# Optimization experiments

Hardware: AMD Instinct MI355X
Metric: run time of the kernel (lower is better)

The kernel has to match this reference:

```python
import jax, jax.numpy as jnp
import numpy as np

H = 4          # heads
C = 64         # per-head channels
HID = 256      # hidden_dim = H*C
L = 4          # num_layers
N = 50000      # nodes
E = 300000     # edges
G = 64         # graphs
NODE_DIMS = [80, 16, 8]
EDGE_DIMS = [8, 4]


def setup_inputs() -> dict:
    key = jax.random.key(0)
    ks = iter(jax.random.split(key, 64))
    def nrm(shape, fan_in):
        return jax.random.normal(next(ks), shape, dtype=jnp.float32) * (1.0 / np.sqrt(fan_in))
    inp = {}
    inp['x'] = jax.random.randint(next(ks), (N, 3), 0, 8)
    inp['edge_attr'] = jax.random.randint(next(ks), (E, 2), 0, 4)
    inp['edge_index'] = jax.random.randint(next(ks), (2, E), 0, N)
    inp['batch'] = jnp.sort(jax.random.randint(next(ks), (N,), 0, G))
    inp['scalars'] = jax.random.uniform(next(ks), (G, 5), dtype=jnp.float32)
    inp['num_graphs'] = G
    # categorical embedding tables (summed per field)
    inp['node_emb0'] = nrm((NODE_DIMS[0], HID), HID)
    inp['node_emb1'] = nrm((NODE_DIMS[1], HID), HID)
    inp['node_emb2'] = nrm((NODE_DIMS[2], HID), HID)
    inp['edge_emb0'] = nrm((EDGE_DIMS[0], HID), HID)
    inp['edge_emb1'] = nrm((EDGE_DIMS[1], HID), HID)
    # stacked per-layer TransformerConv params
    inp['Wq'] = nrm((L, HID, HID), HID); inp['bq'] = jnp.zeros((L, HID))
    inp['Wk'] = nrm((L, HID, HID), HID); inp['bk'] = jnp.zeros((L, HID))
    inp['Wv'] = nrm((L, HID, HID), HID); inp['bv'] = jnp.zeros((L, HID))
    inp['We'] = nrm((L, HID, HID), HID); inp['be'] = jnp.zeros((L, HID))
    inp['Wskip'] = nrm((L, HID, HID), HID); inp['bskip'] = jnp.zeros((L, HID))
    inp['Wbeta'] = nrm((L, 3 * HID, 1), 3 * HID)  # beta gate, bias=False in PyG
    inp['ln_g'] = jnp.ones((L, HID)); inp['ln_b'] = jnp.zeros((L, HID))
    # pragma scalar encoder
    inp['pw1'] = nrm((5, HID), 5); inp['pb1'] = jnp.zeros((HID,))
    inp['pw2'] = nrm((HID, HID), HID); inp['pb2'] = jnp.zeros((HID,))
    # readout MLP
    inp['rw1'] = nrm((HID, HID), HID); inp['rb1'] = jnp.zeros((HID,))
    inp['rw2'] = nrm((HID, HID // 2), HID); inp['rb2'] = jnp.zeros((HID // 2,))
    inp['rw3'] = nrm((HID // 2, 4), HID // 2); inp['rb3'] = jnp.zeros((4,))
    return inp


def _forward(scalars, node_emb0, node_emb1, node_emb2, edge_emb0, edge_emb1,
             Wq, bq, Wk, bk, Wv, bv, We, be, Wskip, bskip, Wbeta, ln_g, ln_b,
             pw1, pb1, pw2, pb2, rw1, rb1, rw2, rb2, rw3, rb3,
             x, edge_attr, edge_index, batch, num_graphs):
    n = x.shape[0]
    src, dst = edge_index[0], edge_index[1]
    # CategoricalEmbedding: sum of per-field embeddings
    h = node_emb0[x[:, 0]] + node_emb1[x[:, 1]] + node_emb2[x[:, 2]]      # [N, HID]
    ef = edge_emb0[edge_attr[:, 0]] + edge_emb1[edge_attr[:, 1]]          # [E, HID]
    scale = 1.0 / jnp.sqrt(jnp.asarray(C, h.dtype))
    for l in range(L):
        q = (h @ Wq[l] + bq[l]).reshape(n, H, C)
        kN = (h @ Wk[l] + bk[l]).reshape(n, H, C)
        vN = (h @ Wv[l] + bv[l]).reshape(n, H, C)
        e = (ef @ We[l] + be[l]).reshape(-1, H, C)                        # [E, H, C]
        kj = kN[src] + e                                                  # edge feat added to keys
        alpha = jnp.sum(q[dst] * kj, axis=-1) * scale                     # [E, H]
        # segment softmax over incoming edges per destination node
        amax = jax.ops.segment_max(alpha, dst, num_segments=n)
        amax = jnp.where(jnp.isfinite(amax), amax, 0.0)
        ea = jnp.exp(alpha - amax[dst])
        denom = jax.ops.segment_sum(ea, dst, num_segments=n)
        attn = ea / jnp.maximum(denom, 1e-16)[dst]                        # [E, H]
        msg = (vN[src] + e) * attn[..., None]                             # edge feat added to values
        out = jax.ops.segment_sum(msg, dst, num_segments=n).reshape(n, HID)
        # beta gated skip (TransformerConv beta=True, root_weight=True)
        r = h @ Wskip[l] + bskip[l]
        beta = jax.nn.sigmoid(jnp.concatenate([out, r, out - r], axis=-1) @ Wbeta[l])  # [N,1]
        out = beta * r + (1.0 - beta) * out
        out = jax.nn.relu(out)
        # LayerNorm over hidden dim
        mu = jnp.mean(out, axis=-1, keepdims=True)
        var = jnp.var(out, axis=-1, keepdims=True)
        out = (out - mu) * jax.lax.rsqrt(var + 1e-5) * ln_g[l] + ln_b[l]
        h = h + out                                                       # residual (dropout off in eval)
    pooled = jax.ops.segment_sum(h, batch, num_segments=num_graphs)       # global_add_pool
    p = jax.nn.relu(scalars @ pw1 + pb1) @ pw2 + pb2                      # pragma encoder
    pooled = pooled + p
    z = jax.nn.relu(pooled @ rw1 + rb1)
    z = jax.nn.relu(z @ rw2 + rb2)
    return z @ rw3 + rb3                                                  # [G, 4]


def reference(x, edge_attr, edge_index, batch, scalars, num_graphs,
              node_emb0, node_emb1, node_emb2, edge_emb0, edge_emb1,
              Wq, bq, Wk, bk, Wv, bv, We, be, Wskip, bskip, Wbeta, ln_g, ln_b,
              pw1, pb1, pw2, pb2, rw1, rb1, rw2, rb2, rw3, rb3):
    return _forward(scalars, node_emb0, node_emb1, node_emb2, edge_emb0, edge_emb1,
                    Wq, bq, Wk, bk, Wv, bv, We, be, Wskip, bskip, Wbeta, ln_g, ln_b,
                    pw1, pb1, pw2, pb2, rw1, rb1, rw2, rb2, rw3, rb3,
                    x, edge_attr, edge_index, batch, num_graphs)
```

## Files before the change

kernel.cpp:

```cpp
#include <hip/hip_runtime.h>
#include <hip/hip_bf16.h>

typedef short short8 __attribute__((ext_vector_type(8)));
typedef float floatx4 __attribute__((ext_vector_type(4)));
typedef float floatx2 __attribute__((ext_vector_type(2)));
typedef __hip_bfloat16 bf16;

#define HID 256
#define NL  4
#define QROW 1536
#define AS1 __attribute__((address_space(1)))
#define AS3 __attribute__((address_space(3)))

__device__ __forceinline__ float b2f(bf16 v) { return __bfloat162float(v); }
__device__ __forceinline__ bf16 f2b(float v) { return __float2bfloat16(v); }
__device__ __forceinline__ float us2f(unsigned short u) {
    unsigned int x = ((unsigned int)u) << 16;
    return __uint_as_float(x);
}
__device__ __forceinline__ unsigned short f2us(float v) {
    bf16 t = __float2bfloat16(v);
    return *reinterpret_cast<unsigned short*>(&t);
}

template <int CTRL>
__device__ __forceinline__ float row_ror_add(float x) {
    return x + __int_as_float(__builtin_amdgcn_update_dpp(
        0, __float_as_int(x), CTRL, 0xF, 0xF, true));
}

__global__ void zero_ws_kernel(int* __restrict__ a, int* __restrict__ b, int n,
                               float* __restrict__ p, int np) {
    int i = blockIdx.x * 256 + threadIdx.x;
    if (i < n) { a[i] = 0; b[i] = 0; }
    if (i < np) p[i] = 0.f;
}

__global__ __launch_bounds__(256) void node_embed_kernel(const int* __restrict__ x,
                                  const float* __restrict__ e0, const float* __restrict__ e1,
                                  const float* __restrict__ e2,
                                  bf16* __restrict__ hbf, int N) {
    const int tid = threadIdx.x;
    const int n = blockIdx.x * 4 + (tid >> 6);
    if (n >= N) return;
    const int c4 = (tid & 63) * 4;
    const int i0 = x[n * 3], i1 = x[n * 3 + 1], i2 = x[n * 3 + 2];
    const float4 a = *reinterpret_cast<const float4*>(e0 + i0 * HID + c4);
    const float4 b = *reinterpret_cast<const float4*>(e1 + i1 * HID + c4);
    const float4 c = *reinterpret_cast<const float4*>(e2 + i2 * HID + c4);
    ushort4 o;
    o.x = f2us(a.x + b.x + c.x);
    o.y = f2us(a.y + b.y + c.y);
    o.z = f2us(a.z + b.z + c.z);
    o.w = f2us(a.w + b.w + c.w);
    *reinterpret_cast<ushort4*>(hbf + (size_t)n * HID + c4) = o;
}

__global__ void ecombo_embed_kernel(const float* __restrict__ e0, const float* __restrict__ e1,
                                    float* __restrict__ ec) {
    int i = blockIdx.x, c = threadIdx.x;
    ec[i * HID + c] = e0[(i >> 2) * HID + c] + e1[(i & 3) * HID + c];
}

__global__ void edge_prep_kernel(const int* __restrict__ ea, const int* __restrict__ dst,
                                 int E, int* __restrict__ ecid, int* __restrict__ counts) {
    int e = blockIdx.x * 256 + threadIdx.x;
    if (e < E) {
        ecid[e] = ea[e * 2] * 4 + ea[e * 2 + 1];
        atomicAdd(&counts[dst[e]], 1);
    }
}

__global__ void combo_proj_kernel(const float* __restrict__ ec, const float* __restrict__ We,
                                  const float* __restrict__ be, float* __restrict__ ecp4) {
    __shared__ float row[HID];
    int l = blockIdx.x >> 5, i = blockIdx.x & 31, c = threadIdx.x;
    row[c] = ec[i * HID + c];
    __syncthreads();
    const float* We_l = We + (size_t)l * 65536;
    float a = be[l * 256 + c];
    for (int k = 0; k < HID; ++k) a += row[k] * We_l[k * HID + c];
    ecp4[(size_t)l * 32 * HID + i * HID + c] = a;
}

__global__ void scan_local_kernel(const int* __restrict__ counts, int N,
                                  int* __restrict__ incl, int* __restrict__ bsum) {
    __shared__ int sd[256];
    int i = threadIdx.x;
    int idx = blockIdx.x * 256 + i;
    sd[i] = (idx < N) ? counts[idx] : 0;
    __syncthreads();
    for (int off = 1; off < 256; off <<= 1) {
        int t = (i >= off) ? sd[i - off] : 0;
        __syncthreads();
        sd[i] += t;
        __syncthreads();
    }
    if (idx < N) incl[idx] = sd[i];
    if (i == 255) bsum[blockIdx.x] = sd[255];
}

__global__ void scan_block_kernel(const int* __restrict__ bsum, int nb, int* __restrict__ boff) {
    __shared__ int sd[256];
    int i = threadIdx.x;
    sd[i] = (i < nb) ? bsum[i] : 0;
    __syncthreads();
    for (int off = 1; off < 256; off <<= 1) {
        int t = (i >= off) ? sd[i - off] : 0;
        __syncthreads();
        sd[i] += t;
        __syncthreads();
    }
    if (i < nb) boff[i] = (i == 0) ? 0 : sd[i - 1];
}

__global__ void scan_add_kernel(const int* __restrict__ incl, const int* __restrict__ boff,
                                int N, int* __restrict__ indptr) {
    int idx = blockIdx.x * 256 + threadIdx.x;
    if (idx < N) indptr[idx + 1] = incl[idx] + boff[blockIdx.x];
    if (idx == 0) indptr[0] = 0;
}

__global__ void fill_sorted_kernel(const int* __restrict__ dst, const int* __restrict__ srcv,
                                   const int* __restrict__ ecid, const int* __restrict__ indptr,
                                   int E, int* __restrict__ fill, int2* __restrict__ sorted2) {
    int e = blockIdx.x * 256 + threadIdx.x;
    if (e < E) {
        int d = dst[e];
        int pos = indptr[d] + atomicAdd(&fill[d], 1);
        sorted2[pos] = make_int2(srcv[e] * QROW, ecid[e] << 10);
    }
    if (e < 4) sorted2[E + e] = make_int2(0, 0);
}

__global__ __launch_bounds__(256) void pack_wcat_kernel(
    const float* __restrict__ Wq, const float* __restrict__ Wk,
    const float* __restrict__ Wv, const float* __restrict__ Ws,
    bf16* __restrict__ wcatT) {
    __shared__ bf16 tile[64][65];
    const int jt = blockIdx.x;
    const int kt = blockIdx.y;
    const int l  = blockIdx.z;
    const int tid = threadIdx.x;
    const int jl = tid & 63;
    const int j = jt * 64 + jl;
    const float* W;
    int jj;
    if (j < 256)      { W = Wq; jj = j; }
    else if (j < 512) { W = Ws; jj = j - 256; }
    else {
        int g = (j - 512) >> 3, r = (j - 512) & 7;
        if (r < 4) { W = Wk; jj = 4 * g + r; }
        else       { W = Wv; jj = 4 * g + r - 4; }
    }
    const float* Wbase = W + (size_t)l * 65536 + jj + (size_t)(kt * 64) * 256;
    const int kr = tid >> 6;
#pragma unroll
    for (int i = 0; i < 16; ++i) {
        const int kl = kr + i * 4;
        tile[kl][jl] = f2b(Wbase[(size_t)kl * 256]);
    }
    __syncthreads();
    const int kl2 = tid & 63;
    const int jr = tid >> 6;
    bf16* out = wcatT + (size_t)l * 262144 + (size_t)(jt * 64) * 256 + kt * 64 + kl2;
#pragma unroll
    for (int i = 0; i < 16; ++i) {
        const int jl2 = jr + i * 4;
        out[(size_t)jl2 * 256] = tile[kl2][jl2];
    }
}

__global__ void pack_bias_kernel(const float* __restrict__ bq, const float* __restrict__ bk,
                                 const float* __restrict__ bv, const float* __restrict__ bs,
                                 float* __restrict__ bcat) {
    int idx = blockIdx.x * 256 + threadIdx.x;
    if (idx < 4096) {
        int l = idx >> 10, j = idx & 1023;
        const float* B;
        int jj;
        if (j < 256)      { B = bq; jj = j; }
        else if (j < 512) { B = bs; jj = j - 256; }
        else {
            int g = (j - 512) >> 3, r = (j - 512) & 7;
            if (r < 4) { B = bk; jj = 4 * g + r; }
            else       { B = bv; jj = 4 * g + r - 4; }
        }
        bcat[idx] = B[l * 256 + jj];
    }
}

__global__ __launch_bounds__(512) void gemm_bt_kernel(
    const bf16* __restrict__ A, const bf16* __restrict__ BT,
    const float* __restrict__ bias, char* __restrict__ Cb, int M) {
    constexpr int BM = 128, BN = 256, BK = 64, CSTR = 136;
    __shared__ __align__(16) bf16 smem[BM * 64 + BN * 64];
    bf16* sA = smem;
    bf16* sB = smem + BM * 64;
    const int m0 = blockIdx.y * BM;
    const int n0 = blockIdx.x * BN;
    const int tid = threadIdx.x;
    const int lane = tid & 63;
    const int wave = tid >> 6;
    const int wm = (wave >> 2) * 64;
    const int wn = (wave & 3) * 64;
    const int fr = lane & 15;
    const int quad = lane >> 4;
    const int sub = lane >> 3;
    const int slot = lane & 7;
    const int jsw = slot ^ sub;
    const bool isfp8 = (n0 >= 512);
    floatx4 acc[4][4] = {};
    for (int kc = 0; kc < 256; kc += BK) {
#pragma unroll
        for (int p = 0; p < 2; ++p) {
            const int brow = (wave * 2 + p) * 8;
            const int gm = min(m0 + brow + sub, M - 1);
            __builtin_amdgcn_global_load_lds(
                (const AS1 void*)(A + (size_t)gm * 256 + kc + jsw * 8),
                (AS3 void*)(sA + brow * 64), 16, 0, 0);
        }
#pragma unroll
        for (int p = 0; p < 4; ++p) {
            const int brow = (wave * 4 + p) * 8;
            __builtin_amdgcn_global_load_lds(
                (const AS1 void*)(BT + (size_t)(n0 + brow + sub) * 256 + kc + jsw * 8),
                (AS3 void*)(sB + brow * 64), 16, 0, 0);
        }
        __syncthreads();
#pragma unroll
        for (int ks = 0; ks < BK; ks += 32) {
            const int ch = (ks >> 3) + quad;
            const int phys = (ch ^ (fr & 7)) << 3;
            short8 af[4], bfm[4];
#pragma unroll
            for (int i = 0; i < 4; ++i) {
                af[i]  = *reinterpret_cast<const short8*>(&sA[(wm + i * 16 + fr) * 64 + phys]);
                bfm[i] = *reinterpret_cast<const short8*>(&sB[(wn + i * 16 + fr) * 64 + phys]);
            }
#pragma unroll
            for (int mi = 0; mi < 4; ++mi)
#pragma unroll
                for (int ni = 0; ni < 4; ++ni)
                    acc[mi][ni] = __builtin_amdgcn_mfma_f32_16x16x32_bf16(af[mi], bfm[ni], acc[mi][ni], 0, 0, 0);
        }
        __syncthreads();
    }
    float bias4[4];
#pragma unroll
    for (int ni = 0; ni < 4; ++ni) bias4[ni] = bias[n0 + wn + ni * 16 + fr];
    bf16* sC = smem;
    const int myhalf = wn >> 7;
#pragma unroll
    for (int half = 0; half < 2; ++half) {
        if (myhalf == half) {
            const int wnl = wn & 127;
#pragma unroll
            for (int mi = 0; mi < 4; ++mi)
#pragma unroll
                for (int ni = 0; ni < 4; ++ni)
#pragma unroll
                    for (int r = 0; r < 4; ++r)
                        sC[(wm + mi * 16 + quad * 4 + r) * CSTR + wnl + ni * 16 + fr] =
                            f2b(acc[mi][ni][r] + bias4[ni]);
        }
        __syncthreads();
#pragma unroll
        for (int p = 0; p < 4; ++p) {
            int ci = tid + p * 512;
            int row = ci >> 4;
            int c8 = (ci & 15) << 3;
            if (m0 + row < M) {
                const uint4 vv = *reinterpret_cast<const uint4*>(&sC[row * CSTR + c8]);
                char* crow = Cb + (size_t)(m0 + row) * QROW;
                const int col = n0 + half * 128 + c8;
                if (!isfp8) {
                    *reinterpret_cast<uint4*>(crow + col * 2) = vv;
                } else {
                    const float f0 = us2f((unsigned short)(vv.x & 0xffff)), f1 = us2f((unsigned short)(vv.x >> 16));
                    const float f2 = us2f((unsigned short)(vv.y & 0xffff)), f3 = us2f((unsigned short)(vv.y >> 16));
                    const float f4 = us2f((unsigned short)(vv.z & 0xffff)), f5 = us2f((unsigned short)(vv.z >> 16));
                    const float f6 = us2f((unsigned short)(vv.w & 0xffff)), f7 = us2f((unsigned short)(vv.w >> 16));
                    int lo = 0, hi = 0;
                    lo = __builtin_amdgcn_cvt_pk_fp8_f32(f0, f1, lo, false);
                    lo = __builtin_amdgcn_cvt_pk_fp8_f32(f2, f3, lo, true);
                    hi = __builtin_amdgcn_cvt_pk_fp8_f32(f4, f5, hi, false);
                    hi = __builtin_amdgcn_cvt_pk_fp8_f32(f6, f7, hi, true);
                    uint2 o;
                    o.x = (unsigned)lo;
                    o.y = (unsigned)hi;
                    *reinterpret_cast<uint2*>(crow + 1024 + (col - 512)) = o;
                }
            }
        }
        __syncthreads();
    }
}

__global__ __launch_bounds__(256) void attn_node_kernel(
    const char* __restrict__ qkvs,
    const float* __restrict__ ecp,
    const int* __restrict__ indptr, const int2* __restrict__ sorted2,
    const float* __restrict__ Wbeta_l, const float* __restrict__ lng, const float* __restrict__ lnb,
    bf16* __restrict__ hbf, int N) {
    const int tid = threadIdx.x;
    const int wv = tid >> 6;
    const int lane = tid & 63;
    const int n = blockIdx.x * 4 + wv;
    if (n >= N) return;
    const int c0 = lane * 4;
    const ushort4 qu = *reinterpret_cast<const ushort4*>(qkvs + (size_t)n * QROW + lane * 8);
    const float q0 = us2f(qu.x), q1 = us2f(qu.y), q2 = us2f(qu.z), q3 = us2f(qu.w);
    float a0 = 0.f, a1 = 0.f, a2 = 0.f, a3 = 0.f, wsum = 0.f;
    const int e0 = indptr[n], e1 = indptr[n + 1];
    const char* __restrict__ kvb = qkvs + 1024 + lane * 8;
    const char* __restrict__ epb = (const char*)ecp + c0 * 4;

    auto edge_body = [&](const uint2& kv, const float4& ep) {
        const floatx2 ka = __builtin_amdgcn_cvt_pk_f32_fp8(kv.x, false);
        const floatx2 kb = __builtin_amdgcn_cvt_pk_f32_fp8(kv.x, true);
        const floatx2 va = __builtin_amdgcn_cvt_pk_f32_fp8(kv.y, false);
        const floatx2 vb = __builtin_amdgcn_cvt_pk_f32_fp8(kv.y, true);
        float t = q0 * (ka.x + ep.x) + q1 * (ka.y + ep.y) + q2 * (kb.x + ep.z) + q3 * (kb.y + ep.w);
        t = row_ror_add<0x121>(t);
        t = row_ror_add<0x122>(t);
        t = row_ror_add<0x124>(t);
        t = row_ror_add<0x128>(t);
        const float w = __expf(t * 0.125f);
        a0 += w * (va.x + ep.x);
        a1 += w * (va.y + ep.y);
        a2 += w * (vb.x + ep.z);
        a3 += w * (vb.y + ep.w);
        wsum += w;
    };

    if (e0 < e1) {
        int2 m0 = sorted2[e0];
        int2 m1 = sorted2[e0 + 1];
        uint2 kv0 = *reinterpret_cast<const uint2*>(kvb + (unsigned)m0.x);
        uint2 kv1 = *reinterpret_cast<const uint2*>(kvb + (unsigned)m1.x);
        int ee = e0;
        for (; ee + 1 < e1; ee += 2) {
            const int2 mN0 = sorted2[ee + 2];
            const int2 mN1 = sorted2[ee + 3];
            const uint2 kvN0 = *reinterpret_cast<const uint2*>(kvb + (unsigned)mN0.x);
            const uint2 kvN1 = *reinterpret_cast<const uint2*>(kvb + (unsigned)mN1.x);
            const float4 ep0 = *reinterpret_cast<const float4*>(epb + (unsigned)m0.y);
            const float4 ep1 = *reinterpret_cast<const float4*>(epb + (unsigned)m1.y);
            edge_body(kv0, ep0);
            edge_body(kv1, ep1);
            m0 = mN0; m1 = mN1;
            kv0 = kvN0; kv1 = kvN1;
        }
        if (ee < e1) {
            const float4 ep0 = *reinterpret_cast<const float4*>(epb + (unsigned)m0.y);
            edge_body(kv0, ep0);
        }
    }
    const float inv = (wsum > 0.f) ? 1.f / wsum : 0.f;
    const float o0 = a0 * inv, o1 = a1 * inv, o2 = a2 * inv, o3 = a3 * inv;
    const ushort4 ru = *reinterpret_cast<const ushort4*>(qkvs + (size_t)n * QROW + 512 + lane * 8);
    const float r0 = us2f(ru.x), r1 = us2f(ru.y), r2 = us2f(ru.z), r3 = us2f(ru.w);
    const float4 w1 = *reinterpret_cast<const float4*>(Wbeta_l + c0);
    const float4 w2 = *reinterpret_cast<const float4*>(Wbeta_l + 256 + c0);
    const float4 w3 = *reinterpret_cast<const float4*>(Wbeta_l + 512 + c0);
    float tb = o0 * w1.x + o1 * w1.y + o2 * w1.z + o3 * w1.w
             + r0 * w2.x + r1 * w2.y + r2 * w2.z + r3 * w2.w
             + (o0 - r0) * w3.x + (o1 - r1) * w3.y + (o2 - r2) * w3.z + (o3 - r3) * w3.w;
#pragma unroll
    for (int off = 32; off > 0; off >>= 1) tb += __shfl_xor(tb, off);
    const float beta = 1.f / (1.f + __expf(-tb));
    float g0 = fmaxf(beta * r0 + (1.f - beta) * o0, 0.f);
    float g1 = fmaxf(beta * r1 + (1.f - beta) * o1, 0.f);
    float g2 = fmaxf(beta * r2 + (1.f - beta) * o2, 0.f);
    float g3 = fmaxf(beta * r3 + (1.f - beta) * o3, 0.f);
    float s1 = g0 + g1 + g2 + g3;
    float s2 = g0 * g0 + g1 * g1 + g2 * g2 + g3 * g3;
#pragma unroll
    for (int off = 32; off > 0; off >>= 1) { s1 += __shfl_xor(s1, off); s2 += __shfl_xor(s2, off); }
    const float mu = s1 * (1.f / 256.f);
    const float var = s2 * (1.f / 256.f) - mu * mu;
    const float rish = rsqrtf(fmaxf(var, 0.f) + 1e-5f);
    const float4 gg = *reinterpret_cast<const float4*>(lng + c0);
    const float4 bb = *reinterpret_cast<const float4*>(lnb + c0);
    ushort4 hb = *reinterpret_cast<ushort4*>(hbf + (size_t)n * HID + c0);
    float h0 = us2f(hb.x) + (g0 - mu) * rish * gg.x + bb.x;
    float h1 = us2f(hb.y) + (g1 - mu) * rish * gg.y + bb.y;
    float h2 = us2f(hb.z) + (g2 - mu) * rish * gg.z + bb.z;
    float h3 = us2f(hb.w) + (g3 - mu) * rish * gg.w + bb.w;
    hb.x = f2us(h0); hb.y = f2us(h1); hb.z = f2us(h2); hb.w = f2us(h3);
    *reinterpret_cast<ushort4*>(hbf + (size_t)n * HID + c0) = hb;
}

__global__ __launch_bounds__(256) void pool_kernel(const bf16* __restrict__ hbf,
                                                   const int* __restrict__ batch,
                                                   float* __restrict__ pooled, int N) {
    __shared__ int sb[64];
    const int c = threadIdx.x;
    const int n0 = blockIdx.x * 64;
    const int cnt = min(64, N - n0);
    if (c < 64 && c < cnt) sb[c] = batch[n0 + c];
    __syncthreads();
    float acc = 0.f;
    int gcur = sb[0];
    for (int i = 0; i < cnt; ++i) {
        const int g = sb[i];
        if (g != gcur) {
            atomicAdd(&pooled[(size_t)gcur * HID + c], acc);
            acc = 0.f;
            gcur = g;
        }
        acc += b2f(hbf[(size_t)(n0 + i) * HID + c]);
    }
    atomicAdd(&pooled[(size_t)gcur * HID + c], acc);
}

__global__ void pragma_kernel(const float* __restrict__ scalars,
                              const float* __restrict__ pw1, const float* __restrict__ pb1,
                              const float* __restrict__ pw2, const float* __restrict__ pb2,
                              float* __restrict__ pooled) {
    int g = blockIdx.x, c = threadIdx.x;
    __shared__ float s5[5];
    __shared__ float t1[256];
    if (c < 5) s5[c] = scalars[g * 5 + c];
    __syncthreads();
    float a = pb1[c];
    for (int k = 0; k < 5; ++k) a += s5[k] * pw1[k * 256 + c];
    t1[c] = fmaxf(a, 0.f);
    __syncthreads();
    float p = pb2[c];
    for (int j = 0; j < 256; ++j) p += t1[j] * pw2[j * 256 + c];
    pooled[g * 256 + c] += p;
}

__global__ void readout_kernel(const float* __restrict__ pooled,
                               const float* __restrict__ rw1, const float* __restrict__ rb1,
                               const float* __restrict__ rw2, const float* __restrict__ rb2,
                               const float* __restrict__ rw3, const float* __restrict__ rb3,
                               float* __restrict__ out) {
    int g = blockIdx.x, c = threadIdx.x;
    __shared__ float pl[256], z1[256], z2[128];
    pl[c] = pooled[g * 256 + c];
    __syncthreads();
    float z = rb1[c];
    for (int k = 0; k < 256; ++k) z += pl[k] * rw1[k * 256 + c];
    z1[c] = fmaxf(z, 0.f);
    __syncthreads();
    if (c < 128) {
        float v = rb2[c];
        for (int j = 0; j < 256; ++j) v += z1[j] * rw2[j * 128 + c];
        z2[c] = fmaxf(v, 0.f);
    }
    __syncthreads();
    if (c < 4) {
        float o = rb3[c];
        for (int j = 0; j < 128; ++j) o += z2[j] * rw3[j * 4 + c];
        out[g * 4 + c] = o;
    }
}

extern "C" void kernel_launch(void* const* d_in, const int* in_sizes, int n_in,
                              void* d_out, int out_size, void* d_ws, size_t ws_size,
                              hipStream_t stream) {
    const int* x          = (const int*)d_in[0];
    const int* edge_attr  = (const int*)d_in[1];
    const int* edge_index = (const int*)d_in[2];
    const int* batch      = (const int*)d_in[3];
    const float* scalars  = (const float*)d_in[4];
    const float* ne0 = (const float*)d_in[6];
    const float* ne1 = (const float*)d_in[7];
    const float* ne2 = (const float*)d_in[8];
    const float* ee0 = (const float*)d_in[9];
    const float* ee1 = (const float*)d_in[10];
    const float* Wq = (const float*)d_in[11];
    const float* bq = (const float*)d_in[12];
    const float* Wk = (const float*)d_in[13];
    const float* bk = (const float*)d_in[14];
    const float* Wv = (const float*)d_in[15];
    const float* bv = (const float*)d_in[16];
    const float* We = (const float*)d_in[17];
    const float* be = (const float*)d_in[18];
    const float* Wskip = (const float*)d_in[19];
    const float* bskip = (const float*)d_in[20];
    const float* Wbeta = (const float*)d_in[21];
    const float* ln_g = (const float*)d_in[22];
    const float* ln_b = (const float*)d_in[23];
    const float* pw1 = (const float*)d_in[24];
    const float* pb1 = (const float*)d_in[25];
    const float* pw2 = (const float*)d_in[26];
    const float* pb2 = (const float*)d_in[27];
    const float* rw1 = (const float*)d_in[28];
    const float* rb1 = (const float*)d_in[29];
    const float* rw2 = (const float*)d_in[30];
    const float* rb2 = (const float*)d_in[31];
    const float* rw3 = (const float*)d_in[32];
    const float* rb3 = (const float*)d_in[33];

    const int N = in_sizes[0] / 3;
    const int E = in_sizes[1] / 2;
    const int G = in_sizes[4] / 5;

    char* base = (char*)d_ws;
    size_t off = 0;
    auto carve = [&](size_t bytes) -> char* {
        char* p = base + off;
        off += (bytes + 255) & ~(size_t)255;
        return p;
    };
    bf16*  hbf    = (bf16*)carve((size_t)N * HID * 2);
    char*  qkvs   = (char*)carve((size_t)N * QROW);
    float* ec     = (float*)carve((size_t)32 * HID * 4);
    float* ecp4   = (float*)carve((size_t)NL * 32 * HID * 4);
    int*   ecid   = (int*)carve((size_t)E * 4);
    float* pooled = (float*)carve((size_t)G * HID * 4);
    bf16*  wcatT  = (bf16*)carve((size_t)NL * 1024 * 256 * 2);
    float* bcat   = (float*)carve((size_t)NL * 1024 * 4);
    int* counts   = (int*)carve((size_t)N * 4);
    int* fill     = (int*)carve((size_t)N * 4);
    int* incl     = (int*)carve((size_t)N * 4);
    int* bsum     = (int*)carve(4096);
    int* boff     = (int*)carve(4096);
    int* indptr   = (int*)carve((size_t)(N + 1) * 4);
    int2* sorted2 = (int2*)carve((size_t)(E + 4) * 8);

    const int* srcv = edge_index;
    const int* dstv = edge_index + E;

    zero_ws_kernel<<<(N + 255) / 256, 256, 0, stream>>>(counts, fill, N, pooled, G * HID);
    node_embed_kernel<<<(N + 3) / 4, 256, 0, stream>>>(x, ne0, ne1, ne2, hbf, N);
    ecombo_embed_kernel<<<32, 256, 0, stream>>>(ee0, ee1, ec);
    edge_prep_kernel<<<(E + 255) / 256, 256, 0, stream>>>(edge_attr, dstv, E, ecid, counts);
    {
        dim3 gp(16, 4, 4);
        pack_wcat_kernel<<<gp, 256, 0, stream>>>(Wq, Wk, Wv, Wskip, wcatT);
    }
    pack_bias_kernel<<<16, 256, 0, stream>>>(bq, bk, bv, bskip, bcat);
    combo_proj_kernel<<<NL * 32, 256, 0, stream>>>(ec, We, be, ecp4);

    int nsb = (N + 255) / 256;
    scan_local_kernel<<<nsb, 256, 0, stream>>>(counts, N, incl, bsum);
    scan_block_kernel<<<1, 256, 0, stream>>>(bsum, nsb, boff);
    scan_add_kernel<<<nsb, 256, 0, stream>>>(incl, boff, N, indptr);
    fill_sorted_kernel<<<(E + 255) / 256, 256, 0, stream>>>(dstv, srcv, ecid, indptr, E, fill, sorted2);

    for (int l = 0; l < NL; ++l) {
        dim3 g1(4, (N + 127) / 128);
        gemm_bt_kernel<<<g1, 512, 0, stream>>>(hbf, wcatT + (size_t)l * 262144,
                                               bcat + (size_t)l * 1024, qkvs, N);
        attn_node_kernel<<<(N + 3) / 4, 256, 0, stream>>>(qkvs, ecp4 + (size_t)l * 32 * HID,
                                                          indptr, sorted2,
                                                          Wbeta + (size_t)l * 768,
                                                          ln_g + (size_t)l * 256, ln_b + (size_t)l * 256,
                                                          hbf, N);
    }

    pool_kernel<<<(N + 63) / 64, 256, 0, stream>>>(hbf, batch, pooled, N);
    pragma_kernel<<<G, 256, 0, stream>>>(scalars, pw1, pb1, pw2, pb2, pooled);
    readout_kernel<<<G, 256, 0, stream>>>(pooled, rw1, rb1, rw2, rb2, rw3, rb3, (float*)d_out);
}
```

Before: 668.9 us.

## Double-buffer QKV GEMM with 128x128 tiles and XCD-aware block mapping

Replaces the 128x256-tile, 512-thread projection GEMM with a 128x128-tile, 256-thread kernel. Each K chunk is loaded into shared memory while the previous chunk is being multiplied, using two ping-pong buffers. A one-dimensional grid is remapped so that all eight N-tiles of one M-tile land on the same XCD, which should improve L2 reuse of the A rows. The goal is to hide global-load latency and raise occupancy (launch bounds 256,2). The cost is that each A row is now loaded by more blocks (8 instead of 4) and the epilogue tile is smaller.

Result: faster. 575.1 us, median of 2 (-14.0%).

```diff
diff --git a/kernel.cpp b/kernel.cpp
--- a/kernel.cpp
+++ b/kernel.cpp
@@ -190,53 +190,65 @@
     }
 }
 
-__global__ __launch_bounds__(512) void gemm_bt_kernel(
+__global__ __launch_bounds__(256, 2) void gemm_db_kernel(
     const bf16* __restrict__ A, const bf16* __restrict__ BT,
     const float* __restrict__ bias, char* __restrict__ Cb, int M) {
-    constexpr int BM = 128, BN = 256, BK = 64, CSTR = 136;
-    __shared__ __align__(16) bf16 smem[BM * 64 + BN * 64];
-    bf16* sA = smem;
-    bf16* sB = smem + BM * 64;
-    const int m0 = blockIdx.y * BM;
-    const int n0 = blockIdx.x * BN;
+    __shared__ __align__(16) bf16 smem[32768];
     const int tid = threadIdx.x;
     const int lane = tid & 63;
     const int wave = tid >> 6;
-    const int wm = (wave >> 2) * 64;
-    const int wn = (wave & 3) * 64;
+    const int mtiles = (M + 127) >> 7;
+    const int q = (mtiles + 7) >> 3;
+    const int d = blockIdx.x;
+    const int xcd = d & 7;
+    const int j = d >> 3;
+    const int mt = xcd * q + (j >> 3);
+    if (mt >= mtiles) return;
+    const int m0 = mt << 7;
+    const int n0 = (j & 7) << 7;
     const int fr = lane & 15;
     const int quad = lane >> 4;
     const int sub = lane >> 3;
     const int slot = lane & 7;
     const int jsw = slot ^ sub;
+    const int wm = (wave >> 1) * 64;
+    const int wn = (wave & 1) * 64;
     const bool isfp8 = (n0 >= 512);
-    floatx4 acc[4][4] = {};
-    for (int kc = 0; kc < 256; kc += BK) {
-#pragma unroll
-        for (int p = 0; p < 2; ++p) {
-            const int brow = (wave * 2 + p) * 8;
+
+    bf16* sA0 = smem;          bf16* sB0 = smem + 8192;
+    bf16* sA1 = smem + 16384;  bf16* sB1 = smem + 24576;
+
+    auto stage = [&](int kc, bf16* sA, bf16* sB) {
+#pragma unroll
+        for (int p = 0; p < 4; ++p) {
+            const int brow = (wave * 4 + p) * 8;
             const int gm = min(m0 + brow + sub, M - 1);
             __builtin_amdgcn_global_load_lds(
                 (const AS1 void*)(A + (size_t)gm * 256 + kc + jsw * 8),
                 (AS3 void*)(sA + brow * 64), 16, 0, 0);
-        }
-#pragma unroll
-        for (int p = 0; p < 4; ++p) {
-            const int brow = (wave * 4 + p) * 8;
             __builtin_amdgcn_global_load_lds(
                 (const AS1 void*)(BT + (size_t)(n0 + brow + sub) * 256 + kc + jsw * 8),
                 (AS3 void*)(sB + brow * 64), 16, 0, 0);
         }
-        __syncthreads();
-#pragma unroll
-        for (int ks = 0; ks < BK; ks += 32) {
+    };
+
+    floatx4 acc[4][4] = {};
+    stage(0, sA0, sB0);
+    __syncthreads();
+#pragma unroll
+    for (int t = 0; t < 4; ++t) {
+        bf16* cA = (t & 1) ? sA1 : sA0;
+        bf16* cB = (t & 1) ? sB1 : sB0;
+        if (t < 3) stage((t + 1) * 64, (t & 1) ? sA0 : sA1, (t & 1) ? sB0 : sB1);
+#pragma unroll
+        for (int ks = 0; ks < 64; ks += 32) {
             const int ch = (ks >> 3) + quad;
             const int phys = (ch ^ (fr & 7)) << 3;
             short8 af[4], bfm[4];
 #pragma unroll
             for (int i = 0; i < 4; ++i) {
-                af[i]  = *reinterpret_cast<const short8*>(&sA[(wm + i * 16 + fr) * 64 + phys]);
-                bfm[i] = *reinterpret_cast<const short8*>(&sB[(wn + i * 16 + fr) * 64 + phys]);
+                af[i]  = *reinterpret_cast<const short8*>(&cA[(wm + i * 16 + fr) * 64 + phys]);
+                bfm[i] = *reinterpret_cast<const short8*>(&cB[(wn + i * 16 + fr) * 64 + phys]);
             }
 #pragma unroll
             for (int mi = 0; mi < 4; ++mi)
@@ -246,54 +258,48 @@
         }
         __syncthreads();
     }
+
     float bias4[4];
 #pragma unroll
     for (int ni = 0; ni < 4; ++ni) bias4[ni] = bias[n0 + wn + ni * 16 + fr];
+    constexpr int CSTR = 136;
     bf16* sC = smem;
-    const int myhalf = wn >> 7;
-#pragma unroll
-    for (int half = 0; half < 2; ++half) {
-        if (myhalf == half) {
-            const int wnl = wn & 127;
-#pragma unroll
-            for (int mi = 0; mi < 4; ++mi)
-#pragma unroll
-                for (int ni = 0; ni < 4; ++ni)
-#pragma unroll
-                    for (int r = 0; r < 4; ++r)
-                        sC[(wm + mi * 16 + quad * 4 + r) * CSTR + wnl + ni * 16 + fr] =
-                            f2b(acc[mi][ni][r] + bias4[ni]);
-        }
-        __syncthreads();
-#pragma unroll
-        for (int p = 0; p < 4; ++p) {
-            int ci = tid + p * 512;
-            int row = ci >> 4;
-            int c8 = (ci & 15) << 3;
-            if (m0 + row < M) {
-                const uint4 vv = *reinterpret_cast<const uint4*>(&sC[row * CSTR + c8]);
-                char* crow = Cb + (size_t)(m0 + row) * QROW;
-                const int col = n0 + half * 128 + c8;
-                if (!isfp8) {
-                    *reinterpret_cast<uint4*>(crow + col * 2) = vv;
-                } else {
-                    const float f0 = us2f((unsigned short)(vv.x & 0xffff)), f1 = us2f((unsigned short)(vv.x >> 16));
-                    const float f2 = us2f((unsigned short)(vv.y & 0xffff)), f3 = us2f((unsigned short)(vv.y >> 16));
-                    const float f4 = us2f((unsigned short)(vv.z & 0xffff)), f5 = us2f((unsigned short)(vv.z >> 16));
-                    const float f6 = us2f((unsigned short)(vv.w & 0xffff)), f7 = us2f((unsigned short)(vv.w >> 16));
-                    int lo = 0, hi = 0;
-                    lo = __builtin_amdgcn_cvt_pk_fp8_f32(f0, f1, lo, false);
-                    lo = __builtin_amdgcn_cvt_pk_fp8_f32(f2, f3, lo, true);
-                    hi = __builtin_amdgcn_cvt_pk_fp8_f32(f4, f5, hi, false);
-                    hi = __builtin_amdgcn_cvt_pk_fp8_f32(f6, f7, hi, true);
-                    uint2 o;
-                    o.x = (unsigned)lo;
-                    o.y = (unsigned)hi;
-                    *reinterpret_cast<uint2*>(crow + 1024 + (col - 512)) = o;
-                }
+#pragma unroll
+    for (int mi = 0; mi < 4; ++mi)
+#pragma unroll
+        for (int ni = 0; ni < 4; ++ni)
+#pragma unroll
+            for (int r = 0; r < 4; ++r)
+                sC[(wm + mi * 16 + quad * 4 + r) * CSTR + wn + ni * 16 + fr] =
+                    f2b(acc[mi][ni][r] + bias4[ni]);
+    __syncthreads();
+#pragma unroll
+    for (int p = 0; p < 8; ++p) {
+        const int ci = tid + p * 256;
+        const int row = ci >> 4;
+        const int c8 = (ci & 15) << 3;
+        if (m0 + row < M) {
+            const uint4 vv = *reinterpret_cast<const uint4*>(&sC[row * CSTR + c8]);
+            char* crow = Cb + (size_t)(m0 + row) * QROW;
+            const int col = n0 + c8;
+            if (!isfp8) {
+                *reinterpret_cast<uint4*>(crow + col * 2) = vv;
+            } else {
+                const float f0 = us2f((unsigned short)(vv.x & 0xffff)), f1 = us2f((unsigned short)(vv.x >> 16));
+                const float f2 = us2f((unsigned short)(vv.y & 0xffff)), f3 = us2f((unsigned short)(vv.y >> 16));
+                const float f4 = us2f((unsigned short)(vv.z & 0xffff)), f5 = us2f((unsigned short)(vv.z >> 16));
+                const float f6 = us2f((unsigned short)(vv.w & 0xffff)), f7 = us2f((unsigned short)(vv.w >> 16));
+                int lo = 0, hi = 0;
+                lo = __builtin_amdgcn_cvt_pk_fp8_f32(f0, f1, lo, false);
+                lo = __builtin_amdgcn_cvt_pk_fp8_f32(f2, f3, lo, true);
+                hi = __builtin_amdgcn_cvt_pk_fp8_f32(f4, f5, hi, false);
+                hi = __builtin_amdgcn_cvt_pk_fp8_f32(f6, f7, hi, true);
+                uint2 o;
+                o.x = (unsigned)lo;
+                o.y = (unsigned)hi;
+                *reinterpret_cast<uint2*>(crow + 1024 + (col - 512)) = o;
             }
         }
-        __syncthreads();
     }
 }
 
@@ -543,10 +549,13 @@
     scan_add_kernel<<<nsb, 256, 0, stream>>>(incl, boff, N, indptr);
     fill_sorted_kernel<<<(E + 255) / 256, 256, 0, stream>>>(dstv, srcv, ecid, indptr, E, fill, sorted2);
 
+    const int mtiles = (N + 127) / 128;
+    const int qx = (mtiles + 7) / 8;
+    const int gemm_grid = 64 * qx;
+
     for (int l = 0; l < NL; ++l) {
-        dim3 g1(4, (N + 127) / 128);
-        gemm_bt_kernel<<<g1, 512, 0, stream>>>(hbf, wcatT + (size_t)l * 262144,
-                                               bcat + (size_t)l * 1024, qkvs, N);
+        gemm_db_kernel<<<gemm_grid, 256, 0, stream>>>(hbf, wcatT + (size_t)l * 262144,
+                                                      bcat + (size_t)l * 1024, qkvs, N);
         attn_node_kernel<<<(N + 3) / 4, 256, 0, stream>>>(qkvs, ecp4 + (size_t)l * 32 * HID,
                                                           indptr, sorted2,
                                                           Wbeta + (size_t)l * 768,
```
